# Performance work log

Hardware: AMD Instinct MI355X
Metric: run time of the kernel (lower is better)

Reference implementation:

```python
import jax, jax.numpy as jnp
import numpy as np

B, S, D, H, L, OUT = 4, 1024, 1024, 16, 6, 512
HD = D // H
EPS = 1e-5


def _positional_encoding(seq, dim):
    pos = np.arange(seq, dtype=np.float32)[:, None]          # [S,1]
    i = np.arange(0, dim, 2, dtype=np.float32)[None, :]       # even indices
    div = np.power(10000.0, 2.0 * i / dim)                    # repo's (nonstandard) exponent
    pe = np.zeros((seq, dim), dtype=np.float32)
    pe[:, 0::2] = np.sin(pos / div)
    pe[:, 1::2] = np.cos(pos / div)
    return jnp.asarray(pe)[None]                               # [1,S,D]


def _causal_mask(seq):
    r = jnp.arange(seq)
    m = jnp.where(r[None, :] > r[:, None], jnp.float32(-jnp.inf), jnp.float32(0.0))
    return m[None, None]                                       # [1,1,S,S]


def setup_inputs() -> dict:
    key = jax.random.key(0)
    ks = jax.random.split(key, 10)
    sc = 0.02
    inp = {
        'x':      jax.random.normal(ks[0], (B, S, D), jnp.float32),
        'pe':     _positional_encoding(S, D),
        'mask':   _causal_mask(S),
        'ln1_g':  jnp.ones((L, D), jnp.float32),
        'ln1_b':  jnp.zeros((L, D), jnp.float32),
        'wq':     jax.random.normal(ks[1], (L, D, D), jnp.float32) * sc,
        'wk':     jax.random.normal(ks[2], (L, D, D), jnp.float32) * sc,
        'wv':     jax.random.normal(ks[3], (L, D, D), jnp.float32) * sc,
        'wo':     jax.random.normal(ks[4], (L, D, D), jnp.float32) * sc,
        'ln2_g':  jnp.ones((L, D), jnp.float32),
        'ln2_b':  jnp.zeros((L, D), jnp.float32),
        'wf':     jax.random.normal(ks[5], (L, D, D), jnp.float32) * sc,
        'lnf_g':  jnp.ones((D,), jnp.float32),
        'lnf_b':  jnp.zeros((D,), jnp.float32),
        'w_out':  jax.random.normal(ks[6], (OUT, D), jnp.float32) * sc,
    }
    return inp


def _layer_norm(x, g, b):
    mu = jnp.mean(x, axis=-1, keepdims=True)
    var = jnp.mean(jnp.square(x - mu), axis=-1, keepdims=True)
    return (x - mu) * jax.lax.rsqrt(var + EPS) * g + b


def _split_heads(x):
    b, s, d = x.shape
    return x.reshape(b, s, H, HD).transpose(0, 2, 1, 3)  # [B,H,S,HD]


def reference(x, pe, mask, ln1_g, ln1_b, wq, wk, wv, wo, ln2_g, ln2_b, wf, lnf_g, lnf_b, w_out):
    h = x + pe
    scale = 1.0 / jnp.sqrt(jnp.float32(HD))
    for l in range(wq.shape[0]):
        h_ = _layer_norm(h, ln1_g[l], ln1_b[l])
        q = _split_heads(jnp.einsum('bsd,ed->bse', h_, wq[l]))
        k = _split_heads(jnp.einsum('bsd,ed->bse', h_, wk[l]))
        v = _split_heads(jnp.einsum('bsd,ed->bse', h_, wv[l]))
        scores = jnp.einsum('bhqd,bhkd->bhqk', q, k) * scale + mask  # [B,H,S,S]
        probs = jax.nn.softmax(scores, axis=-1)
        attn = jnp.einsum('bhqk,bhkd->bhqd', probs, v)
        attn = attn.transpose(0, 2, 1, 3).reshape(h.shape)            # combine heads
        h = h + jnp.einsum('bsd,ed->bse', attn, wo[l])
        h_ = _layer_norm(h, ln2_g[l], ln2_b[l])
        h = h + jnp.einsum('bsd,ed->bse', h_, wf[l])                  # FFN = plain linear (no activation, as in source)
    h = _layer_norm(h, lnf_g, lnf_b)
    return jnp.einsum('bsd,od->bso', h, w_out)
```

## Files before the change

### kernel.cpp

```cpp
#include <hip/hip_runtime.h>
#include <hip/hip_bf16.h>
#include <stdint.h>

#define BATCH 4
#define SEQ   1024
#define DIM   1024
#define NH    16
#define HDIM  64
#define NLAYER 6
#define NOUT  512
#define NTOK  (BATCH*SEQ)
#define LOG2E 1.44269504088896f
#define NEG_BIG (-1e30f)
#define VTS   72

using bf16 = __hip_bfloat16;
typedef __attribute__((ext_vector_type(4))) float f32x4;
typedef __attribute__((ext_vector_type(8))) short bf16x8;

typedef __attribute__((address_space(1))) void as1_void;
typedef __attribute__((address_space(3))) void as3_void;

__device__ __forceinline__ float bf2f(short u) {
  union { unsigned int i; float f; } c;
  c.i = ((unsigned int)(unsigned short)u) << 16;
  return c.f;
}

__device__ __forceinline__ short f2bs(float f) {
  bf16 h = __float2bfloat16(f);
  return *(short*)&h;
}

__device__ __forceinline__ float exp_clamped(float x) {
  return exp2f(fmaxf(x, -100.f) * LOG2E);
}

__device__ __forceinline__ float loadf(const void* p, size_t i, bool f32) {
  return f32 ? ((const float*)p)[i] : __bfloat162float(((const bf16*)p)[i]);
}

__device__ __forceinline__ void g2l16(const void* g, void* l) {
  __builtin_amdgcn_global_load_lds((const as1_void*)g, (as3_void*)l, 16, 0, 0);
}

__global__ void sniff(const unsigned int* __restrict__ w, int* __restrict__ flag) {
  const int lane = threadIdx.x;
  const unsigned int word = w[lane];
  const int e2 = (word >> 7) & 0xFF;
  const bool bf16ish = (e2 >= 0x60) && (e2 <= 0x8F);
  const unsigned long long m = __ballot(bf16ish);
  if (lane == 0) *flag = (__popcll(m) >= 48) ? 0 : 1;
}

__global__ __launch_bounds__(256) void convert_w(const void* __restrict__ src,
                                                 bf16* __restrict__ dst,
                                                 const int* __restrict__ flag) {
  const size_t i = ((size_t)blockIdx.x * 256 + threadIdx.x) * 8;
  if (*flag) {
    const float* s = (const float*)src + i;
#pragma unroll
    for (int e = 0; e < 8; ++e) dst[i + e] = __float2bfloat16(s[e]);
  } else {
    *(bf16x8*)(dst + i) = *(const bf16x8*)((const bf16*)src + i);
  }
}

template<int EPI>
__device__ __forceinline__ void gemm_body(const bf16* __restrict__ A,
                                          const bf16* __restrict__ W,
                                          void* __restrict__ C,
                                          const int* __restrict__ flag,
                                          int N, int m0, int n0) {
  __shared__ __align__(16) bf16 lA[128 * 32];
  __shared__ __align__(16) bf16 lB[128 * 32];
  const int tid  = threadIdx.x;
  const int wave = tid >> 6;
  const int lane = tid & 63;
  const int quad = lane >> 4;
  const int l16  = lane & 15;
  const int wm = (wave >> 1) * 64;
  const int wn = (wave & 1) * 64;
  const int K = DIM;

  const int r0 = tid >> 2;
  const int c0 = (tid & 3) * 8;
  const int r1 = (tid + 256) >> 2;

  bool f32out = false;
  if (EPI == 2) f32out = (*flag != 0);

  f32x4 acc[4][4];
#pragma unroll
  for (int i = 0; i < 4; ++i)
#pragma unroll
    for (int j = 0; j < 4; ++j) acc[i][j] = (f32x4){0.f, 0.f, 0.f, 0.f};

  for (int k0 = 0; k0 < K; k0 += 32) {
    __syncthreads();
    g2l16(A + (size_t)(m0 + r0) * K + k0 + c0, lA + 512 * wave);
    g2l16(A + (size_t)(m0 + r1) * K + k0 + c0, lA + 2048 + 512 * wave);
    g2l16(W + (size_t)(n0 + r0) * K + k0 + c0, lB + 512 * wave);
    g2l16(W + (size_t)(n0 + r1) * K + k0 + c0, lB + 2048 + 512 * wave);
    __builtin_amdgcn_s_waitcnt(0);
    __syncthreads();

    bf16x8 af[4], bfr[4];
#pragma unroll
    for (int i = 0; i < 4; ++i) {
      af[i]  = *(const bf16x8*)(lA + (wm + i * 16 + l16) * 32 + quad * 8);
      bfr[i] = *(const bf16x8*)(lB + (wn + i * 16 + l16) * 32 + quad * 8);
    }
#pragma unroll
    for (int i = 0; i < 4; ++i)
#pragma unroll
      for (int j = 0; j < 4; ++j)
        acc[i][j] = __builtin_amdgcn_mfma_f32_16x16x32_bf16(af[i], bfr[j], acc[i][j], 0, 0, 0);
  }

#pragma unroll
  for (int i = 0; i < 4; ++i) {
    const int rowb = m0 + wm + i * 16 + quad * 4;
#pragma unroll
    for (int j = 0; j < 4; ++j) {
      const int col = n0 + wn + j * 16 + l16;
#pragma unroll
      for (int r = 0; r < 4; ++r) {
        const size_t idx = (size_t)(rowb + r) * N + col;
        const float v = acc[i][j][r];
        if (EPI == 0) ((bf16*)C)[idx] = __float2bfloat16(v);
        else { if (f32out) ((float*)C)[idx] = v; else ((bf16*)C)[idx] = __float2bfloat16(v); }
      }
    }
  }
}

__device__ __forceinline__ void gemm64_body(const bf16* __restrict__ A,
                                            const bf16* __restrict__ W,
                                            float* __restrict__ C,
                                            int N, int m0, int n0) {
  __shared__ __align__(16) bf16 lA[64 * 32];
  __shared__ __align__(16) bf16 lB[128 * 32];
  const int tid  = threadIdx.x;
  const int wave = tid >> 6;
  const int lane = tid & 63;
  const int quad = lane >> 4;
  const int l16  = lane & 15;
  const int wm = (wave >> 1) * 32;
  const int wn = (wave & 1) * 64;
  const int K = DIM;

  const int r0 = tid >> 2;
  const int c0 = (tid & 3) * 8;
  const int r1 = (tid + 256) >> 2;

  f32x4 acc[2][4];
#pragma unroll
  for (int i = 0; i < 2; ++i)
#pragma unroll
    for (int j = 0; j < 4; ++j) acc[i][j] = (f32x4){0.f, 0.f, 0.f, 0.f};

  for (int k0 = 0; k0 < K; k0 += 32) {
    __syncthreads();
    g2l16(A + (size_t)(m0 + r0) * K + k0 + c0, lA + 512 * wave);
    g2l16(W + (size_t)(n0 + r0) * K + k0 + c0, lB + 512 * wave);
    g2l16(W + (size_t)(n0 + r1) * K + k0 + c0, lB + 2048 + 512 * wave);
    __builtin_amdgcn_s_waitcnt(0);
    __syncthreads();

    bf16x8 af[2], bfr[4];
#pragma unroll
    for (int i = 0; i < 2; ++i)
      af[i]  = *(const bf16x8*)(lA + (wm + i * 16 + l16) * 32 + quad * 8);
#pragma unroll
    for (int j = 0; j < 4; ++j)
      bfr[j] = *(const bf16x8*)(lB + (wn + j * 16 + l16) * 32 + quad * 8);
#pragma unroll
    for (int i = 0; i < 2; ++i)
#pragma unroll
      for (int j = 0; j < 4; ++j)
        acc[i][j] = __builtin_amdgcn_mfma_f32_16x16x32_bf16(af[i], bfr[j], acc[i][j], 0, 0, 0);
  }

#pragma unroll
  for (int i = 0; i < 2; ++i) {
    const int rowb = m0 + wm + i * 16 + quad * 4;
#pragma unroll
    for (int j = 0; j < 4; ++j) {
      const int col = n0 + wn + j * 16 + l16;
#pragma unroll
      for (int r = 0; r < 4; ++r)
        C[(size_t)(rowb + r) * N + col] += acc[i][j][r];
    }
  }
}

__global__ __launch_bounds__(256) void gemm_out(const bf16* __restrict__ A,
                                                const bf16* __restrict__ W,
                                                void* __restrict__ C,
                                                const int* __restrict__ flag) {
  gemm_body<2>(A, W, C, flag, NOUT, blockIdx.y * 128, blockIdx.x * 128);
}

__global__ __launch_bounds__(256) void gemm_add(const bf16* __restrict__ A,
                                                const bf16* __restrict__ W,
                                                float* __restrict__ C) {
  gemm64_body(A, W, C, DIM, blockIdx.y * 64, blockIdx.x * 128);
}

__global__ __launch_bounds__(256) void gemm_qkv(const bf16* __restrict__ A,
                                                const bf16* __restrict__ wq,
                                                const bf16* __restrict__ wk,
                                                const bf16* __restrict__ wv,
                                                bf16* __restrict__ q,
                                                bf16* __restrict__ k,
                                                bf16* __restrict__ v) {
  const int gx = blockIdx.x;
  const int sel = gx >> 3;
  const int n0 = (gx & 7) * 128;
  const bf16* W = (sel == 0) ? wq : (sel == 1 ? wk : wv);
  bf16* C = (sel == 0) ? q : (sel == 1 ? k : v);
  gemm_body<0>(A, W, C, nullptr, DIM, blockIdx.y * 128, n0);
}

__global__ __launch_bounds__(256) void add_pe(const void* __restrict__ x,
                                              const void* __restrict__ pe,
                                              float* __restrict__ h,
                                              const int* __restrict__ flag) {
  const bool f32 = (*flag != 0);
  const size_t i = (size_t)blockIdx.x * 256 + threadIdx.x;
  h[i] = loadf(x, i, f32) + loadf(pe, i & (SEQ * DIM - 1), f32);
}

__global__ __launch_bounds__(256) void layernorm(const float* __restrict__ x,
                                                 const void* __restrict__ g,
                                                 const void* __restrict__ b,
                                                 int loff,
                                                 bf16* __restrict__ y,
                                                 const int* __restrict__ flag) {
  const bool f32 = (*flag != 0);
  const int row = blockIdx.x;
  const int tid = threadIdx.x;
  const int wave = tid >> 6;
  const float* xr = x + (size_t)row * DIM;
  __shared__ float red[8];

  float v[4];
  float s = 0.f;
#pragma unroll
  for (int i = 0; i < 4; ++i) { v[i] = xr[tid + 256 * i]; s += v[i]; }
#pragma unroll
  for (int off = 32; off >= 1; off >>= 1) s += __shfl_xor(s, off);
  if ((tid & 63) == 0) red[wave] = s;
  __syncthreads();
  const float mu = (red[0] + red[1] + red[2] + red[3]) * (1.f / DIM);

  float vs = 0.f;
#pragma unroll
  for (int i = 0; i < 4; ++i) { const float d = v[i] - mu; vs += d * d; }
#pragma unroll
  for (int off = 32; off >= 1; off >>= 1) vs += __shfl_xor(vs, off);
  if ((tid & 63) == 0) red[4 + wave] = vs;
  __syncthreads();
  const float var = (red[4] + red[5] + red[6] + red[7]) * (1.f / DIM);
  const float rs = rsqrtf(var + 1e-5f);

#pragma unroll
  for (int i = 0; i < 4; ++i) {
    const int d = tid + 256 * i;
    const float gv = loadf(g, (size_t)loff + d, f32);
    const float bv = loadf(b, (size_t)loff + d, f32);
    y[(size_t)row * DIM + d] = __float2bfloat16((v[i] - mu) * rs * gv + bv);
  }
}

__global__ __launch_bounds__(256, 2) void attn_flash(const bf16* __restrict__ q,
                                                     const bf16* __restrict__ k,
                                                     const bf16* __restrict__ v,
                                                     bf16* __restrict__ o) {
  __shared__ __align__(16) short lK[64 * 64];
  __shared__ __align__(16) short lVT[64 * VTS];
  __shared__ __align__(16) short lP[4 * 16 * VTS];

  const int idx = blockIdx.x;
  const int qt = (SEQ / 64 - 1) - (idx >> 6);
  const int bh = idx & 63;
  const int hh = bh & (NH - 1);
  const int bb = bh >> 4;
  const int q0 = qt * 64;

  const int tid = threadIdx.x;
  const int wave = tid >> 6;
  const int lane = tid & 63;
  const int quad = lane >> 4;
  const int l16 = lane & 15;

  const size_t base = (size_t)bb * SEQ * DIM + hh * HDIM;
  const int qlo = q0 + wave * 16;

  bf16x8 qf[2];
  {
    const bf16* qr = q + base + (size_t)(qlo + l16) * DIM;
#pragma unroll
    for (int kc = 0; kc < 2; ++kc) {
      bf16x8 t = *(const bf16x8*)(qr + kc * 32 + quad * 8);
      bf16x8 sq;
#pragma unroll
      for (int e = 0; e < 8; ++e) sq[e] = f2bs(bf2f(t[e]) * 0.125f);
      qf[kc] = sq;
    }
  }

  float l_acc[4] = {0.f, 0.f, 0.f, 0.f};
  f32x4 oacc[4];
#pragma unroll
  for (int nb = 0; nb < 4; ++nb) oacc[nb] = (f32x4){0.f, 0.f, 0.f, 0.f};

  short* lPw = lP + wave * 16 * VTS;
  const int nt = qt + 1;

  for (int t = 0; t < nt; ++t) {
    const int kbase = t * 64;
    __syncthreads();

    {
      const int r8 = lane >> 3;
      const int cc = (lane & 7) ^ r8;
#pragma unroll
      for (int c = 0; c < 2; ++c) {
        const int row = wave * 16 + c * 8 + r8;
        g2l16(k + base + (size_t)(kbase + row) * DIM + cc * 8,
              lK + (wave * 16 + c * 8) * 64);
      }
    }

    bf16x8 vch[2];
#pragma unroll
    for (int c2 = 0; c2 < 2; ++c2) {
      const int cid = tid + c2 * 256;
      const int kk = cid >> 3;
      const int d0 = (cid & 7) * 8;
      vch[c2] = *(const bf16x8*)(v + base + (size_t)(kbase + kk) * DIM + d0);
    }
#pragma unroll
    for (int c2 = 0; c2 < 2; ++c2) {
      const int cid = tid + c2 * 256;
      const int kk = cid >> 3;
      const int d0 = (cid & 7) * 8;
#pragma unroll
      for (int e = 0; e < 8; ++e) {
        const int d = d0 + e;
        const int kks = kk ^ (((d >> 3) & 7) << 3);
        lVT[d * VTS + kks] = vch[c2][e];
      }
    }
    __builtin_amdgcn_s_waitcnt(0);
    __syncthreads();

    f32x4 s[4];
#pragma unroll
    for (int nb = 0; nb < 4; ++nb) {
      f32x4 acc = (f32x4){0.f, 0.f, 0.f, 0.f};
      const int n = nb * 16 + l16;
#pragma unroll
      for (int kc = 0; kc < 2; ++kc) {
        const int cidx = (kc * 4 + quad) ^ (n & 7);
        bf16x8 kf = *(const bf16x8*)(lK + n * 64 + cidx * 8);
        acc = __builtin_amdgcn_mfma_f32_16x16x32_bf16(qf[kc], kf, acc, 0, 0, 0);
      }
      s[nb] = acc;
    }

    if (kbase + 63 > qlo) {
#pragma unroll
      for (int nb = 0; nb < 4; ++nb) {
        const int j = kbase + nb * 16 + l16;
#pragma unroll
        for (int r = 0; r < 4; ++r)
          if (j > qlo + quad * 4 + r) s[nb][r] = NEG_BIG;
      }
    }

#pragma unroll
    for (int nb = 0; nb < 4; ++nb) {
#pragma unroll
      for (int r = 0; r < 4; ++r) {
        const float p = exp_clamped(s[nb][r]);
        l_acc[r] += p;
        lPw[(quad * 4 + r) * VTS + nb * 16 + l16] = f2bs(p);
      }
    }

    __builtin_amdgcn_s_waitcnt(0);
    bf16x8 pf[2];
#pragma unroll
    for (int kc = 0; kc < 2; ++kc)
      pf[kc] = *(const bf16x8*)(lPw + l16 * VTS + kc * 32 + quad * 8);

#pragma unroll
    for (int nb = 0; nb < 4; ++nb) {
      const int n = nb * 16 + l16;
      const int swz = ((n >> 3) & 7) << 3;
#pragma unroll
      for (int kc = 0; kc < 2; ++kc) {
        const int kchunk = (kc * 32 + quad * 8) ^ swz;
        bf16x8 vf = *(const bf16x8*)(lVT + n * VTS + kchunk);
        oacc[nb] = __builtin_amdgcn_mfma_f32_16x16x32_bf16(pf[kc], vf, oacc[nb], 0, 0, 0);
      }
    }
  }

  float linv[4];
#pragma unroll
  for (int r = 0; r < 4; ++r) {
    float ts = l_acc[r];
#pragma unroll
    for (int off = 8; off >= 1; off >>= 1) ts += __shfl_xor(ts, off);
    linv[r] = 1.f / ts;
  }
#pragma unroll
  for (int nb = 0; nb < 4; ++nb)
#pragma unroll
    for (int r = 0; r < 4; ++r) {
      const int qrow = q0 + wave * 16 + quad * 4 + r;
      o[base + (size_t)qrow * DIM + nb * 16 + l16] =
          __float2bfloat16(oacc[nb][r] * linv[r]);
    }
}

extern "C" void kernel_launch(void* const* d_in, const int* in_sizes, int n_in,
                              void* d_out, int out_size, void* d_ws, size_t ws_size,
                              hipStream_t stream) {
  const void* x    = d_in[0];
  const void* pe   = d_in[1];
  const void* ln1g = d_in[3];
  const void* ln1b = d_in[4];
  const void* wq   = d_in[5];
  const void* wk   = d_in[6];
  const void* wv   = d_in[7];
  const void* wo   = d_in[8];
  const void* ln2g = d_in[9];
  const void* ln2b = d_in[10];
  const void* wf   = d_in[11];
  const void* lnfg = d_in[12];
  const void* lnfb = d_in[13];
  const void* wout = d_in[14];

  const size_t MB = 1u << 20;
  char* ws = (char*)d_ws;
  int*  flag = (int*)ws;
  bf16* wqc  = (bf16*)(ws + 1 * MB);
  bf16* wkc  = (bf16*)(ws + 13 * MB);
  bf16* wvc  = (bf16*)(ws + 25 * MB);
  bf16* woc  = (bf16*)(ws + 37 * MB);
  bf16* wfc  = (bf16*)(ws + 49 * MB);
  bf16* woutc= (bf16*)(ws + 61 * MB);
  float* h   = (float*)(ws + 62 * MB);
  bf16* hn   = (bf16*)(ws + 78 * MB);
  bf16* qb   = (bf16*)(ws + 86 * MB);
  bf16* kb   = (bf16*)(ws + 94 * MB);
  bf16* vb   = (bf16*)(ws + 102 * MB);
  bf16* ab   = hn;

  sniff<<<1, 64, 0, stream>>>((const unsigned int*)wq, flag);

  const int WBLK = (NLAYER * DIM * DIM) / (256 * 8);
  convert_w<<<WBLK, 256, 0, stream>>>(wq, wqc, flag);
  convert_w<<<WBLK, 256, 0, stream>>>(wk, wkc, flag);
  convert_w<<<WBLK, 256, 0, stream>>>(wv, wvc, flag);
  convert_w<<<WBLK, 256, 0, stream>>>(wo, woc, flag);
  convert_w<<<WBLK, 256, 0, stream>>>(wf, wfc, flag);
  convert_w<<<(NOUT * DIM) / (256 * 8), 256, 0, stream>>>(wout, woutc, flag);

  add_pe<<<NTOK * DIM / 256, 256, 0, stream>>>(x, pe, h, flag);

  for (int l = 0; l < NLAYER; ++l) {
    const size_t woff = (size_t)l << 20;
    const int poff = l * DIM;
    layernorm<<<NTOK, 256, 0, stream>>>(h, ln1g, ln1b, poff, hn, flag);
    gemm_qkv<<<dim3(24, 32), 256, 0, stream>>>(hn, wqc + woff, wkc + woff, wvc + woff,
                                               qb, kb, vb);
    attn_flash<<<dim3(BATCH * NH * (SEQ / 64)), 256, 0, stream>>>(qb, kb, vb, ab);
    gemm_add<<<dim3(8, 64), 256, 0, stream>>>(ab, woc + woff, h);
    layernorm<<<NTOK, 256, 0, stream>>>(h, ln2g, ln2b, poff, hn, flag);
    gemm_add<<<dim3(8, 64), 256, 0, stream>>>(hn, wfc + woff, h);
  }

  layernorm<<<NTOK, 256, 0, stream>>>(h, lnfg, lnfb, 0, hn, flag);
  gemm_out<<<dim3(4, 32), 256, 0, stream>>>(hn, woutc, d_out, flag);
}
```

Measured before the change: 968.6 us.

## Replace QKV GEMM with 256x256-tile, 8-wave, 4-stage pipelined kernel

Swaps the 128x128-tile QKV projection GEMM for a new kernel that uses 256x256 output tiles, 512 threads, and a 4-deep ring of LDS buffers filled by direct global-to-LDS loads. Fragment reads use an XOR swizzle, and the MFMA work is split into two half-steps with barriers, raised wave priority, and staggered A/B prefetch. The aim is to raise arithmetic intensity and hide global memory latency behind MFMA work. In exchange the grid shrinks to 192 blocks, which may under-fill the GPU's compute units, and each block uses a large amount of LDS.

Result: no change. 982.7 us (+1.5%).

```diff
diff --git a/kernel.cpp b/kernel.cpp
--- a/kernel.cpp
+++ b/kernel.cpp
@@ -208,19 +208,129 @@
   gemm64_body(A, W, C, DIM, blockIdx.y * 64, blockIdx.x * 128);
 }
 
-__global__ __launch_bounds__(256) void gemm_qkv(const bf16* __restrict__ A,
-                                                const bf16* __restrict__ wq,
-                                                const bf16* __restrict__ wk,
-                                                const bf16* __restrict__ wv,
-                                                bf16* __restrict__ q,
-                                                bf16* __restrict__ k,
-                                                bf16* __restrict__ v) {
-  const int gx = blockIdx.x;
-  const int sel = gx >> 3;
-  const int n0 = (gx & 7) * 128;
+__device__ __forceinline__ bf16x8 rd_frag(const short* slab, int row, int quad) {
+  const int g  = row >> 1;
+  const int cc = (((row & 1) << 2) | quad) ^ (g & 7);
+  return *(const bf16x8*)(slab + g * 64 + cc * 8);
+}
+
+__global__ __launch_bounds__(512, 2) void gemm_qkv_8p(const bf16* __restrict__ A,
+                                                      const bf16* __restrict__ wq,
+                                                      const bf16* __restrict__ wk,
+                                                      const bf16* __restrict__ wv,
+                                                      bf16* __restrict__ q,
+                                                      bf16* __restrict__ k,
+                                                      bf16* __restrict__ v) {
+  __shared__ __align__(16) short lA[4 * 8192];
+  __shared__ __align__(16) short lB[4 * 8192];
+
+  const int bid = blockIdx.x;
+  const int mt  = bid / 12;
+  const int rm  = bid - mt * 12;
+  const int sel = rm >> 2;
+  const int n0  = (rm & 3) * 256;
+  const int m0  = mt * 256;
   const bf16* W = (sel == 0) ? wq : (sel == 1 ? wk : wv);
-  bf16* C = (sel == 0) ? q : (sel == 1 ? k : v);
-  gemm_body<0>(A, W, C, nullptr, DIM, blockIdx.y * 128, n0);
+  bf16* C       = (sel == 0) ? q  : (sel == 1 ? k  : v);
+
+  const int tid  = threadIdx.x;
+  const int wave = tid >> 6;
+  const int lane = tid & 63;
+  const int quad = lane >> 4;
+  const int l16  = lane & 15;
+  const int wr   = wave >> 2;
+  const int wc   = wave & 3;
+
+  const int c3   = (lane & 7) ^ (lane >> 3);
+  const int sq   = c3 & 3;
+  const int rsub = ((lane >> 3) << 1) | (c3 >> 2);
+  const size_t aOff0 = (size_t)(m0 + wave * 32 + rsub) * DIM + sq * 8;
+  const size_t aOff1 = aOff0 + (size_t)16 * DIM;
+  const size_t bOff0 = (size_t)(n0 + wave * 32 + rsub) * DIM + sq * 8;
+  const size_t bOff1 = bOff0 + (size_t)16 * DIM;
+  const int ldsW = wave * 1024;
+
+#define STAGE_A8(J) { short* s_ = lA + ((J) & 3) * 8192 + ldsW;                 \
+    g2l16(A + aOff0 + (J) * 32, s_); g2l16(A + aOff1 + (J) * 32, s_ + 512); }
+#define STAGE_B8(J) { short* s_ = lB + ((J) & 3) * 8192 + ldsW;                 \
+    g2l16(W + bOff0 + (J) * 32, s_); g2l16(W + bOff1 + (J) * 32, s_ + 512); }
+
+  f32x4 acc[8][4];
+#pragma unroll
+  for (int i = 0; i < 8; ++i)
+#pragma unroll
+    for (int jn = 0; jn < 4; ++jn) acc[i][jn] = (f32x4){0.f, 0.f, 0.f, 0.f};
+
+  STAGE_A8(0); STAGE_B8(0);
+  STAGE_A8(1); STAGE_B8(1);
+  STAGE_A8(2); STAGE_B8(2);
+  STAGE_B8(3);
+  asm volatile("s_waitcnt vmcnt(6)" ::: "memory");
+  __builtin_amdgcn_s_barrier();
+  __builtin_amdgcn_sched_barrier(0);
+
+  const int arow = wr * 128 + l16;
+  const int brow = wc * 64 + l16;
+
+  for (int jo = 0; jo < 32; jo += 4) {
+#pragma unroll
+    for (int ji = 0; ji < 4; ++ji) {
+      const int j = jo + ji;
+      const short* sA = lA + ji * 8192;
+      const short* sB = lB + ji * 8192;
+      bf16x8 af[4], bfv[4];
+#pragma unroll
+      for (int mi = 0; mi < 4; ++mi) af[mi]  = rd_frag(sA, arow + mi * 16, quad);
+#pragma unroll
+      for (int nj = 0; nj < 4; ++nj) bfv[nj] = rd_frag(sB, brow + nj * 16, quad);
+      if (j < 29) STAGE_A8(j + 3);
+      __builtin_amdgcn_s_barrier();
+      asm volatile("s_waitcnt lgkmcnt(0)" ::: "memory");
+      __builtin_amdgcn_sched_barrier(0);
+      __builtin_amdgcn_s_setprio(1);
+#pragma unroll
+      for (int mi = 0; mi < 4; ++mi)
+#pragma unroll
+        for (int nj = 0; nj < 4; ++nj)
+          acc[mi][nj] = __builtin_amdgcn_mfma_f32_16x16x32_bf16(af[mi], bfv[nj], acc[mi][nj], 0, 0, 0);
+      __builtin_amdgcn_s_setprio(0);
+      __builtin_amdgcn_s_barrier();
+      __builtin_amdgcn_sched_barrier(0);
+#pragma unroll
+      for (int mi = 0; mi < 4; ++mi) af[mi] = rd_frag(sA, arow + 64 + mi * 16, quad);
+      if (j < 28) STAGE_B8(j + 4);
+      __builtin_amdgcn_s_barrier();
+      asm volatile("s_waitcnt lgkmcnt(0)" ::: "memory");
+      __builtin_amdgcn_sched_barrier(0);
+      __builtin_amdgcn_s_setprio(1);
+#pragma unroll
+      for (int mi = 0; mi < 4; ++mi)
+#pragma unroll
+        for (int nj = 0; nj < 4; ++nj)
+          acc[4 + mi][nj] = __builtin_amdgcn_mfma_f32_16x16x32_bf16(af[mi], bfv[nj], acc[4 + mi][nj], 0, 0, 0);
+      __builtin_amdgcn_s_setprio(0);
+      if (ji & 1) {
+        if (j < 28) { asm volatile("s_waitcnt vmcnt(6)" ::: "memory"); }
+        else        { asm volatile("s_waitcnt vmcnt(0)" ::: "memory"); }
+      }
+      __builtin_amdgcn_s_barrier();
+      __builtin_amdgcn_sched_barrier(0);
+    }
+  }
+#undef STAGE_A8
+#undef STAGE_B8
+
+#pragma unroll
+  for (int mi = 0; mi < 8; ++mi) {
+    const int rowb = m0 + wr * 128 + mi * 16 + quad * 4;
+#pragma unroll
+    for (int nj = 0; nj < 4; ++nj) {
+      const int col = n0 + wc * 64 + nj * 16 + l16;
+#pragma unroll
+      for (int rr = 0; rr < 4; ++rr)
+        C[(size_t)(rowb + rr) * DIM + col] = __float2bfloat16(acc[mi][nj][rr]);
+    }
+  }
 }
 
 __global__ __launch_bounds__(256) void add_pe(const void* __restrict__ x,
@@ -478,7 +588,7 @@
     const size_t woff = (size_t)l << 20;
     const int poff = l * DIM;
     layernorm<<<NTOK, 256, 0, stream>>>(h, ln1g, ln1b, poff, hn, flag);
-    gemm_qkv<<<dim3(24, 32), 256, 0, stream>>>(hn, wqc + woff, wkc + woff, wvc + woff,
+    gemm_qkv_8p<<<dim3(192), 512, 0, stream>>>(hn, wqc + woff, wkc + woff, wvc + woff,
                                                qb, kb, vb);
     attn_flash<<<dim3(BATCH * NH * (SEQ / 64)), 256, 0, stream>>>(qb, kb, vb, ab);
     gemm_add<<<dim3(8, 64), 256, 0, stream>>>(ab, woc + woff, h);
```
